# Kernel optimization log

Hardware: AMD Instinct MI355X
Metric: run time of the kernel (lower is better)

## Reference

```python
import jax, jax.numpy as jnp
import numpy as np


def _rule_stack(x_q):
    # x_q: [B, 2, 4]; a/b are the two context panels, per attribute column -> [B, 4]
    a = x_q[:, 0, :]
    b = x_q[:, 1, :]
    # 13 fixed rules applied elementwise across the 4 attribute columns -> [B, 4, 13]
    return jnp.stack([
        a,
        b - 2.0, b - 1.0, b + 1.0, b + 2.0,
        a - b, a + b,
        jnp.minimum(a, b), jnp.maximum(a, b),
        b + 2.0, b + 1.0, b - 2.0, b - 1.0,
    ], axis=-1)


def setup_inputs() -> dict:
    key = jax.random.key(0)
    k1, k2, k3, k4 = jax.random.split(key, 4)
    B, Z = 262144, 512
    z = jax.random.normal(k1, (B, Z), dtype=jnp.float32)
    x_q = jax.random.normal(k2, (B, 2, 4), dtype=jnp.float32)
    # rule_encoder: Linear(z_dim -> 4*13)
    W = jax.random.normal(k3, (Z, 52), dtype=jnp.float32) / np.sqrt(Z)
    b = jax.random.normal(k4, (52,), dtype=jnp.float32) * 0.01
    return {"z": z, "x_q": x_q, "W": W, "b": b}


def reference(z, x_q, W, b):
    logits = (z @ W + b).reshape(-1, 4, 13)          # [B, 4, 13]
    rule_probs = jax.nn.softmax(logits, axis=-1)       # [B, 4, 13]
    rules = _rule_stack(x_q)                           # [B, 4, 13]
    y_q = jnp.sum(rules * rule_probs, axis=-1)         # [B, 4]
    return y_q[:, None, :]                             # [B, 1, 4]
```

## Files before the change

kernel.cpp:

```cpp
#include <hip/hip_runtime.h>
#include <stdint.h>

typedef __bf16 bf16_t;
typedef bf16_t bf16x8 __attribute__((ext_vector_type(8)));
typedef float f32x4 __attribute__((ext_vector_type(4)));
typedef uint32_t u32x4 __attribute__((ext_vector_type(4)));
typedef uint16_t u16x8 __attribute__((ext_vector_type(8)));

union FragU { u32x4 u; bf16x8 v; u16x8 s; };

__device__ __forceinline__ uint16_t f2bf_rne(float f) {
  uint32_t u = __float_as_uint(f);
  return (uint16_t)((u + 0x7fffu + ((u >> 16) & 1u)) >> 16);
}

__global__ __launch_bounds__(256) void pack_w_kernel(
    const float* __restrict__ W, u32x4* __restrict__ wf) {
  int idx = blockIdx.x * 256 + threadIdx.x;
  if (idx >= 4096) return;
  int lane = idx & 63;
  int nt   = (idx >> 6) & 3;
  int ks   = idx >> 8;
  int n  = nt * 16 + (lane & 15);
  int kb = ks * 32 + (lane >> 4) * 8;
  FragU hi;
#pragma unroll
  for (int j = 0; j < 8; ++j) {
    float w = (n < 52) ? W[(kb + j) * 52 + n] : 0.0f;
    hi.s[j] = f2bf_rne(w);
  }
  wf[idx] = hi.u;
}

#define MFMA16(a, b, c) __builtin_amdgcn_mfma_f32_16x16x32_bf16((a), (b), (c), 0, 0, 0)

__global__ __launch_bounds__(256, 4) void raven_main_kernel(
    const float* __restrict__ z, const float* __restrict__ xq,
    const u32x4* __restrict__ wfh,
    const float* __restrict__ bias, float* __restrict__ out) {
  __shared__ __align__(16) unsigned char smem[33280];
  __shared__ float lds_bias[52];

  const int tid  = threadIdx.x;
  const int wave = tid >> 6;
  const int lane = tid & 63;
  const int r  = lane & 15;
  const int kg = lane >> 4;

  if (tid < 52) lds_bias[tid] = bias[tid];

  const long long brow = (long long)blockIdx.x * 128;
  const long long wrow = brow + (long long)wave * 32;
  const float* zb = z + wrow * 512;

  unsigned char* stg = smem + wave * 8192;

  const int rloc = lane >> 3;
  const int foff = 4 * ((lane & 7) ^ rloc);

  f32x4 acc[2][4];
#pragma unroll
  for (int mt = 0; mt < 2; ++mt)
#pragma unroll
    for (int nt = 0; nt < 4; ++nt) {
      f32x4 zv = {0.0f, 0.0f, 0.0f, 0.0f};
      acc[mt][nt] = zv;
    }

#define STAGE_CHUNK(ks_, buf_)                                                  \
  {                                                                             \
    const float* g_ = zb + rloc * 512 + (ks_) * 32 + foff;                      \
    _Pragma("unroll")                                                           \
    for (int i_ = 0; i_ < 4; ++i_)                                              \
      __builtin_amdgcn_global_load_lds(                                         \
          (const __attribute__((address_space(1))) void*)(g_ + i_ * 8 * 512),   \
          (__attribute__((address_space(3))) void*)((buf_) + i_ * 1024),        \
          16, 0, 0);                                                            \
  }

#define LOADB(ks_, set_)                                                        \
  {                                                                             \
    const u32x4* ph_ = wfh + (ks_) * 256 + lane;                                \
    _Pragma("unroll")                                                           \
    for (int nt_ = 0; nt_ < 4; ++nt_) {                                         \
      bh[set_][nt_].u = ph_[nt_ * 64];                                          \
    }                                                                           \
  }

  FragU bh[2][4];

  LOADB(0, 0);
  STAGE_CHUNK(0, stg);
  LOADB(1, 1);
  STAGE_CHUNK(1, stg + 4096);

  const int swz = (r & 7) << 4;

#pragma unroll
  for (int ks = 0; ks < 16; ++ks) {
    unsigned char* cur = stg + (ks & 1) * 4096;

    if (ks < 15) asm volatile("s_waitcnt vmcnt(8)" ::: "memory");
    else         asm volatile("s_waitcnt vmcnt(0)" ::: "memory");
    __builtin_amdgcn_sched_barrier(0);

    const unsigned char* c0 = cur + r * 128;
    const unsigned char* c1 = cur + (r + 16) * 128;
    f32x4 a00 = *(const f32x4*)(c0 + ((kg * 32) ^ swz));
    f32x4 a01 = *(const f32x4*)(c0 + ((kg * 32 + 16) ^ swz));
    f32x4 a10 = *(const f32x4*)(c1 + ((kg * 32) ^ swz));
    f32x4 a11 = *(const f32x4*)(c1 + ((kg * 32 + 16) ^ swz));

    FragU h0, h1;
#pragma unroll
    for (int j = 0; j < 4; ++j) {
      h0.v[j]     = (bf16_t)a00[j];
      h0.v[4 + j] = (bf16_t)a01[j];
      h1.v[j]     = (bf16_t)a10[j];
      h1.v[4 + j] = (bf16_t)a11[j];
    }

    const int cs = ks & 1;
#pragma unroll
    for (int nt = 0; nt < 4; ++nt) {
      acc[0][nt] = MFMA16(h0.v, bh[cs][nt].v, acc[0][nt]);
      acc[1][nt] = MFMA16(h1.v, bh[cs][nt].v, acc[1][nt]);
    }
    __builtin_amdgcn_sched_barrier(0);

    if (ks < 14) {
      LOADB(ks + 2, cs);
      STAGE_CHUNK(ks + 2, cur);
    }
  }
#undef STAGE_CHUNK
#undef LOADB

  __syncthreads();

  float (*lds)[65] = (float(*)[65])smem;

#pragma unroll
  for (int mt = 0; mt < 2; ++mt)
#pragma unroll
    for (int nt = 0; nt < 4; ++nt)
#pragma unroll
      for (int i = 0; i < 4; ++i)
        lds[wave * 32 + mt * 16 + kg * 4 + i][nt * 16 + r] = acc[mt][nt][i];

  __syncthreads();

  if (tid < 128) {
    int row = tid;
    long long grow = brow + row;
    f32x4 xa = *(const f32x4*)(xq + grow * 8);
    f32x4 xb = *(const f32x4*)(xq + grow * 8 + 4);
    f32x4 res;
#pragma unroll
    for (int g = 0; g < 4; ++g) {
      float a  = xa[g];
      float bq = xb[g];
      float l[13];
      float m = -1e30f;
#pragma unroll
      for (int u = 0; u < 13; ++u) {
        l[u] = lds[row][g * 13 + u] + lds_bias[g * 13 + u];
        m = fmaxf(m, l[u]);
      }
      float s = 0.0f;
#pragma unroll
      for (int u = 0; u < 13; ++u) {
        float e = __expf(l[u] - m);
        l[u] = e;
        s += e;
      }
      float num = a * l[0]
                + (bq - 2.0f) * (l[1] + l[11])
                + (bq - 1.0f) * (l[2] + l[12])
                + (bq + 1.0f) * (l[3] + l[10])
                + (bq + 2.0f) * (l[4] + l[9])
                + (a - bq) * l[5]
                + (a + bq) * l[6]
                + fminf(a, bq) * l[7]
                + fmaxf(a, bq) * l[8];
      res[g] = num / s;
    }
    *(f32x4*)(out + grow * 4) = res;
  }
}

extern "C" void kernel_launch(void* const* d_in, const int* in_sizes, int n_in,
                              void* d_out, int out_size, void* d_ws, size_t ws_size,
                              hipStream_t stream) {
  const float* z    = (const float*)d_in[0];
  const float* xq   = (const float*)d_in[1];
  const float* W    = (const float*)d_in[2];
  const float* bias = (const float*)d_in[3];
  float* out = (float*)d_out;

  const int B = in_sizes[0] / 512;

  u32x4* wf = (u32x4*)d_ws;

  hipLaunchKernelGGL(pack_w_kernel, dim3(16), dim3(256), 0, stream, W, wf);

  const int blocks = B / 128;
  hipLaunchKernelGGL(raven_main_kernel, dim3(blocks), dim3(256), 0, stream,
                     z, xq, (const u32x4*)wf, bias, out);
}
```

Baseline: 108.4 us.

## Split K across waves with 32-row blocks and LDS partial-sum reduction

Each block now handles 32 rows instead of 128. Each of the four waves covers one 128-wide K slice for all 32 rows and stages its whole slice into LDS in a single burst rather than double-buffering 32-column chunks. Partial accumulators are written to LDS in a transposed layout and summed across waves during the softmax epilogue. This gives four times as many blocks and more memory requests in flight per wave. The cost is 64KB of LDS per block, which lowers occupancy to 2 blocks per CU, plus an extra cross-wave reduction, and only 32 threads do the epilogue.

```diff
diff --git a/kernel.cpp b/kernel.cpp
--- a/kernel.cpp
+++ b/kernel.cpp
@@ -34,11 +34,11 @@
 
 #define MFMA16(a, b, c) __builtin_amdgcn_mfma_f32_16x16x32_bf16((a), (b), (c), 0, 0, 0)
 
-__global__ __launch_bounds__(256, 4) void raven_main_kernel(
+__global__ __launch_bounds__(256, 2) void raven_main_kernel(
     const float* __restrict__ z, const float* __restrict__ xq,
     const u32x4* __restrict__ wfh,
     const float* __restrict__ bias, float* __restrict__ out) {
-  __shared__ __align__(16) unsigned char smem[33280];
+  __shared__ __align__(16) unsigned char smem[65536];
   __shared__ float lds_bias[52];
 
   const int tid  = threadIdx.x;
@@ -49,14 +49,11 @@
 
   if (tid < 52) lds_bias[tid] = bias[tid];
 
-  const long long brow = (long long)blockIdx.x * 128;
-  const long long wrow = brow + (long long)wave * 32;
-  const float* zb = z + wrow * 512;
+  const long long brow = (long long)blockIdx.x * 32;
+  const float* zb = z + brow * 512;
 
-  unsigned char* stg = smem + wave * 8192;
-
-  const int rloc = lane >> 3;
-  const int foff = 4 * ((lane & 7) ^ rloc);
+  unsigned char* stgw = smem + wave * 16384;
+  const int wslice = wave * 128;
 
   f32x4 acc[2][4];
 #pragma unroll
@@ -67,92 +64,80 @@
       acc[mt][nt] = zv;
     }
 
-#define STAGE_CHUNK(ks_, buf_)                                                  \
-  {                                                                             \
-    const float* g_ = zb + rloc * 512 + (ks_) * 32 + foff;                      \
-    _Pragma("unroll")                                                           \
-    for (int i_ = 0; i_ < 4; ++i_)                                              \
-      __builtin_amdgcn_global_load_lds(                                         \
-          (const __attribute__((address_space(1))) void*)(g_ + i_ * 8 * 512),   \
-          (__attribute__((address_space(3))) void*)((buf_) + i_ * 1024),        \
-          16, 0, 0);                                                            \
+  {
+    const int rsub = lane >> 5;
+    const int slot = lane & 31;
+#pragma unroll
+    for (int i = 0; i < 16; ++i) {
+      const int ri = i * 2 + rsub;
+      const float* src = zb + ri * 512 + wslice + 4 * (slot ^ (ri & 7));
+      __builtin_amdgcn_global_load_lds(
+          (const __attribute__((address_space(1))) void*)src,
+          (__attribute__((address_space(3))) void*)(stgw + i * 1024),
+          16, 0, 0);
+    }
   }
 
-#define LOADB(ks_, set_)                                                        \
+#define LOADB(kc_, set_)                                                        \
   {                                                                             \
-    const u32x4* ph_ = wfh + (ks_) * 256 + lane;                                \
+    const u32x4* p_ = wfh + (kc_) * 256 + lane;                                 \
     _Pragma("unroll")                                                           \
-    for (int nt_ = 0; nt_ < 4; ++nt_) {                                         \
-      bh[set_][nt_].u = ph_[nt_ * 64];                                          \
-    }                                                                           \
+    for (int nt_ = 0; nt_ < 4; ++nt_)                                           \
+      bh[set_][nt_].u = p_[nt_ * 64];                                           \
   }
 
   FragU bh[2][4];
-
-  LOADB(0, 0);
-  STAGE_CHUNK(0, stg);
-  LOADB(1, 1);
-  STAGE_CHUNK(1, stg + 4096);
+  const int kb0 = wave * 4;
+  LOADB(kb0, 0);
+  LOADB(kb0 + 1, 1);
 
   const int swz = (r & 7) << 4;
 
 #pragma unroll
-  for (int ks = 0; ks < 16; ++ks) {
-    unsigned char* cur = stg + (ks & 1) * 4096;
-
-    if (ks < 15) asm volatile("s_waitcnt vmcnt(8)" ::: "memory");
-    else         asm volatile("s_waitcnt vmcnt(0)" ::: "memory");
+  for (int c = 0; c < 4; ++c) {
+    if (c < 3) asm volatile("s_waitcnt vmcnt(4)" ::: "memory");
+    else       asm volatile("s_waitcnt vmcnt(0)" ::: "memory");
     __builtin_amdgcn_sched_barrier(0);
 
-    const unsigned char* c0 = cur + r * 128;
-    const unsigned char* c1 = cur + (r + 16) * 128;
-    f32x4 a00 = *(const f32x4*)(c0 + ((kg * 32) ^ swz));
-    f32x4 a01 = *(const f32x4*)(c0 + ((kg * 32 + 16) ^ swz));
-    f32x4 a10 = *(const f32x4*)(c1 + ((kg * 32) ^ swz));
-    f32x4 a11 = *(const f32x4*)(c1 + ((kg * 32 + 16) ^ swz));
-
-    FragU h0, h1;
+    FragU h[2];
 #pragma unroll
-    for (int j = 0; j < 4; ++j) {
-      h0.v[j]     = (bf16_t)a00[j];
-      h0.v[4 + j] = (bf16_t)a01[j];
-      h1.v[j]     = (bf16_t)a10[j];
-      h1.v[4 + j] = (bf16_t)a11[j];
+    for (int mt = 0; mt < 2; ++mt) {
+      const unsigned char* cm = stgw + (mt * 16 + r) * 512;
+      f32x4 a0 = *(const f32x4*)(cm + ((c * 128 + kg * 32) ^ swz));
+      f32x4 a1 = *(const f32x4*)(cm + ((c * 128 + kg * 32 + 16) ^ swz));
+#pragma unroll
+      for (int j = 0; j < 4; ++j) {
+        h[mt].v[j]     = (bf16_t)a0[j];
+        h[mt].v[4 + j] = (bf16_t)a1[j];
+      }
     }
 
-    const int cs = ks & 1;
+    const int cs = c & 1;
 #pragma unroll
     for (int nt = 0; nt < 4; ++nt) {
-      acc[0][nt] = MFMA16(h0.v, bh[cs][nt].v, acc[0][nt]);
-      acc[1][nt] = MFMA16(h1.v, bh[cs][nt].v, acc[1][nt]);
+      acc[0][nt] = MFMA16(h[0].v, bh[cs][nt].v, acc[0][nt]);
+      acc[1][nt] = MFMA16(h[1].v, bh[cs][nt].v, acc[1][nt]);
     }
     __builtin_amdgcn_sched_barrier(0);
 
-    if (ks < 14) {
-      LOADB(ks + 2, cs);
-      STAGE_CHUNK(ks + 2, cur);
-    }
+    if (c < 2) LOADB(kb0 + c + 2, cs);
   }
-#undef STAGE_CHUNK
 #undef LOADB
 
   __syncthreads();
 
-  float (*lds)[65] = (float(*)[65])smem;
-
+  float (*ptl)[64][36] = (float(*)[64][36])smem;
 #pragma unroll
   for (int mt = 0; mt < 2; ++mt)
 #pragma unroll
     for (int nt = 0; nt < 4; ++nt)
-#pragma unroll
-      for (int i = 0; i < 4; ++i)
-        lds[wave * 32 + mt * 16 + kg * 4 + i][nt * 16 + r] = acc[mt][nt][i];
+      *(f32x4*)&ptl[wave][nt * 16 + r][mt * 16 + kg * 4] = acc[mt][nt];
 
   __syncthreads();
 
-  if (tid < 128) {
-    int row = tid;
-    long long grow = brow + row;
+  if (tid < 32) {
+    const int row = tid;
+    const long long grow = brow + row;
     f32x4 xa = *(const f32x4*)(xq + grow * 8);
     f32x4 xb = *(const f32x4*)(xq + grow * 8 + 4);
     f32x4 res;
@@ -164,7 +149,9 @@
       float m = -1e30f;
 #pragma unroll
       for (int u = 0; u < 13; ++u) {
-        l[u] = lds[row][g * 13 + u] + lds_bias[g * 13 + u];
+        const int col = g * 13 + u;
+        l[u] = (ptl[0][col][row] + ptl[1][col][row])
+             + (ptl[2][col][row] + ptl[3][col][row]) + lds_bias[col];
         m = fmaxf(m, l[u]);
       }
       float s = 0.0f;
@@ -204,7 +191,7 @@
 
   hipLaunchKernelGGL(pack_w_kernel, dim3(16), dim3(256), 0, stream, W, wf);
 
-  const int blocks = B / 128;
+  const int blocks = B / 32;
   hipLaunchKernelGGL(raven_main_kernel, dim3(blocks), dim3(256), 0, stream,
                      z, xq, (const u32x4*)wf, bias, out);
 }
```

Result: slower. 126.4 us (+16.6%).
